# Kernel tuning notes

Measured on AMD Instinct MI355X. Metric: run time of the kernel, lower is better.

Reference implementation:

```python
import jax, jax.numpy as jnp
import numpy as np

# AttentiveErasing hyperparameters (module defaults)
FILL = 0.0
P = 0.5
MIN_FACTOR = 0.0
MAX_FACTOR = 0.5
MIN_H = 4
MIN_W = 4

B, C, H, W = 512, 1, 224, 224


def setup_inputs() -> dict:
    key = jax.random.key(0)
    # x are attention maps in [0,1]; they are used as bernoulli probabilities.
    x = jax.random.uniform(key, (B, C, H, W), dtype=jnp.float32)
    return {"x": x}


def _per_sample_mask(xmap, factor, key):
    # xmap: [H, W] single-channel attention map for one sample
    h_dim, w_dim = xmap.shape
    k_apply, k_h, k_w = jax.random.split(key, 3)
    apply_flag = jax.random.uniform(k_apply) < P  # torch.rand(1) < p

    flat = xmap.reshape(-1)
    c = jnp.argmax(flat)                 # topk(.,1) center
    cy, cx = c // w_dim, c % w_dim
    mx = flat[c]
    mn = jnp.min(flat)
    thr = mx - (mx - mn) * factor
    prop = xmap > thr                    # proposal region

    ridx = jnp.arange(h_dim)
    cidx = jnp.arange(w_dim)
    rows = jnp.any(prop, axis=1)
    cols = jnp.any(prop, axis=0)
    any_prop = jnp.any(prop)             # empty proposals (factor==0) -> torch raises -> skip
    miny = jnp.min(jnp.where(rows, ridx, h_dim))
    maxy = jnp.max(jnp.where(rows, ridx, -1))
    minx = jnp.min(jnp.where(cols, cidx, w_dim))
    maxx = jnp.max(jnp.where(cols, cidx, -1))
    mh2 = (maxy - miny) // 2
    mw2 = (maxx - minx) // 2
    # torch.randint(min, max//2) raises when max//2 <= min -> except: pass -> skip sample
    valid = any_prop & (mh2 > MIN_H) & (mw2 > MIN_W)

    h = MIN_H + (jax.random.uniform(k_h) * jnp.maximum(mh2 - MIN_H, 1)).astype(jnp.int32)
    w = MIN_W + (jax.random.uniform(k_w) * jnp.maximum(mw2 - MIN_W, 1)).astype(jnp.int32)

    h_start = jnp.maximum(cy - h, 0)
    h_end = jnp.minimum(cy + h, w_dim)   # bug preserved: source clamps height with x.size(3)
    w_start = jnp.maximum(cx - w, 0)
    w_end = jnp.minimum(cx + w, w_dim)

    yy = ridx[:, None]
    xx = cidx[None, :]
    # keep proposal iff strictly inside window AND both coords nonzero (y*x > 0 in source)
    erase = (prop & (yy > h_start) & (yy < h_end)
             & (xx > w_start) & (xx < w_end) & (yy > 0) & (xx > 0))
    do = apply_flag & valid
    return jnp.where(do & erase, FILL, 1.0).astype(xmap.dtype)


def _forward(x):
    b = x.shape[0]
    root = jax.random.key(42)
    k_factor, k_samples, k_noise = jax.random.split(root, 3)
    factor = jax.random.uniform(k_factor, minval=MIN_FACTOR, maxval=MAX_FACTOR)
    keys = jax.random.split(k_samples, b)
    mask2d = jax.vmap(lambda xm, k: _per_sample_mask(xm, factor, k))(x[:, 0], keys)
    mask = mask2d[:, None, :, :]          # [B,1,H,W]

    inp = 0.6 * x + 0.2                   # Dropout input; values in [0.2, 0.8]
    keep_prob = jnp.clip(1.0 - jax.lax.stop_gradient(inp), 0.0, 1.0)
    prob_mask = jax.random.bernoulli(k_noise, keep_prob).astype(x.dtype)
    noise = (1.0 - mask) * prob_mask + mask  # region_mask==1 -> keep; ==0 -> bernoulli
    out = inp * noise
    return out, mask


def reference(x):
    return _forward(x)
```

## Files before the change

### kernel.cpp

```cpp
#include <hip/hip_runtime.h>
#include <cstdint>

typedef unsigned int u32;
typedef float vf4 __attribute__((ext_vector_type(4)));

#define TF_R4(a,b,r1,r2,r3,r4) \
  a += b; b = (b<<r1)|(b>>(32-r1)); b ^= a; \
  a += b; b = (b<<r2)|(b>>(32-r2)); b ^= a; \
  a += b; b = (b<<r3)|(b>>(32-r3)); b ^= a; \
  a += b; b = (b<<r4)|(b>>(32-r4)); b ^= a;

__host__ __device__ inline void tf2x32(u32 k0, u32 k1, u32& x0, u32& x1) {
  const u32 k2 = k0 ^ k1 ^ 0x1BD11BDAu;
  u32 a = x0 + k0, b = x1 + k1;
  TF_R4(a,b,13,15,26,6)   a += k1; b += k2 + 1u;
  TF_R4(a,b,17,29,16,24)  a += k2; b += k0 + 2u;
  TF_R4(a,b,13,15,26,6)   a += k0; b += k1 + 3u;
  TF_R4(a,b,17,29,16,24)  a += k1; b += k2 + 4u;
  TF_R4(a,b,13,15,26,6)   a += k2; b += k0 + 5u;
  x0 = a; x1 = b;
}

__host__ __device__ inline float u01(u32 bits) {
  union { u32 u; float f; } c; c.u = (bits >> 9) | 0x3f800000u;
  return c.f - 1.0f;
}
__host__ __device__ inline u32 rbits_scalar(u32 k0, u32 k1) {
  u32 a = 0, b = 0; tf2x32(k0, k1, a, b); return a ^ b;
}

#define BATCH   512
#define HW      224
#define S       50176
#define NTOT    25690112
#define APB     49
#define FSTR    1152

struct SP { float thr; int hs, he, wss, wee, doit; int pad0, pad1; };
struct AMask { unsigned long long m[8]; };

__global__ __launch_bounds__(256) void k_stats(const float* __restrict__ x,
                                               float* __restrict__ fdata,
                                               AMask am) {
  const int bid = blockIdx.x;
  const int b = bid >> 2, q = bid & 3;
  if (!((am.m[b >> 6] >> (b & 63)) & 1ull)) return;

  const int t = threadIdx.x;
  const int lane = t & 63, wv = t >> 6;
  const float* __restrict__ xs = x + (size_t)b * S;
  float* __restrict__ base = fdata + (size_t)b * FSTR;
  const bool act = lane < 56;

  vf4 cmax = (vf4){0.f, 0.f, 0.f, 0.f};
  float amax = -1.f; int aidx = 0x7fffffff; float amin = 2.f;

#pragma unroll
  for (int k = 0; k < 14; ++k) {
    const int r = q * 56 + wv * 14 + k;
    vf4 v = (vf4){-1.f, -1.f, -1.f, -1.f};
    if (act) v = ((const vf4*)(xs + (size_t)r * HW))[lane];
    float rv = fmaxf(fmaxf(v[0], v[1]), fmaxf(v[2], v[3]));
    if (act) {
      cmax[0] = fmaxf(cmax[0], v[0]); cmax[1] = fmaxf(cmax[1], v[1]);
      cmax[2] = fmaxf(cmax[2], v[2]); cmax[3] = fmaxf(cmax[3], v[3]);
      const int fb = r * HW + lane * 4;
      if (v[0] > amax) { amax = v[0]; aidx = fb; }
      if (v[1] > amax) { amax = v[1]; aidx = fb + 1; }
      if (v[2] > amax) { amax = v[2]; aidx = fb + 2; }
      if (v[3] > amax) { amax = v[3]; aidx = fb + 3; }
      amin = fminf(amin, fminf(fminf(v[0], v[1]), fminf(v[2], v[3])));
    }
    for (int off = 32; off; off >>= 1) rv = fmaxf(rv, __shfl_xor(rv, off));
    if (lane == 0) base[r] = rv;
  }
  for (int off = 32; off; off >>= 1) {
    float v2 = __shfl_xor(amax, off);
    int   i2 = __shfl_xor(aidx, off);
    float n2 = __shfl_xor(amin, off);
    if (v2 > amax || (v2 == amax && i2 < aidx)) { amax = v2; aidx = i2; }
    amin = fminf(amin, n2);
  }
  __shared__ vf4 cmw[4][56];
  __shared__ float wmx[4]; __shared__ int wix[4]; __shared__ float wmn[4];
  if (act) cmw[wv][lane] = cmax;
  if (lane == 0) { wmx[wv] = amax; wix[wv] = aidx; wmn[wv] = amin; }
  __syncthreads();
  if (t < 56) {
    vf4 a = cmw[0][t], c1 = cmw[1][t], c2 = cmw[2][t], c3 = cmw[3][t];
    vf4 m;
    m[0] = fmaxf(fmaxf(a[0], c1[0]), fmaxf(c2[0], c3[0]));
    m[1] = fmaxf(fmaxf(a[1], c1[1]), fmaxf(c2[1], c3[1]));
    m[2] = fmaxf(fmaxf(a[2], c1[2]), fmaxf(c2[2], c3[2]));
    m[3] = fmaxf(fmaxf(a[3], c1[3]), fmaxf(c2[3], c3[3]));
    ((vf4*)(base + 224 + q * 224))[t] = m;
  }
  if (t == 0) {
    float mx = wmx[0]; int ix = wix[0]; float mn = wmn[0];
    for (int wI = 1; wI < 4; ++wI) {
      if (wmx[wI] > mx || (wmx[wI] == mx && wix[wI] < ix)) { mx = wmx[wI]; ix = wix[wI]; }
      mn = fminf(mn, wmn[wI]);
    }
    base[1120 + q * 3 + 0] = mx;
    base[1120 + q * 3 + 1] = __int_as_float(ix);
    base[1120 + q * 3 + 2] = mn;
  }
}

__global__ __launch_bounds__(256) void k_box(const float* __restrict__ fdata,
                                             SP* __restrict__ sp,
                                             float factor, u32 ks0, u32 ks1,
                                             AMask am) {
  const int b = blockIdx.x;
  const int t = threadIdx.x;
  const int lane = t & 63, wv = t >> 6;

  if (!((am.m[b >> 6] >> (b & 63)) & 1ull)) {
    if (t == 0) {
      SP p; p.thr = 0.f; p.hs = 0; p.he = 0; p.wss = 0; p.wee = 0;
      p.doit = 0; p.pad0 = 0; p.pad1 = 0;
      sp[b] = p;
    }
    return;
  }

  const float* __restrict__ base = fdata + (size_t)b * FSTR;
  __shared__ float sc_thr; __shared__ int sc_ix;
  __shared__ int r0[4], r1[4], r2[4], r3[4];

  if (t == 0) {
    float mx = -1.f; int ix = 0x7fffffff; float mn = 2.f;
#pragma unroll
    for (int q2 = 0; q2 < 4; ++q2) {
      const float v = base[1120 + q2 * 3 + 0];
      const int   i = __float_as_int(base[1120 + q2 * 3 + 1]);
      const float n = base[1120 + q2 * 3 + 2];
      if (v > mx || (v == mx && i < ix)) { mx = v; ix = i; }
      mn = fminf(mn, n);
    }
    sc_thr = __fsub_rn(mx, __fmul_rn(__fsub_rn(mx, mn), factor));
    sc_ix = ix;
  }
  __syncthreads();
  const float thr = sc_thr;

  int miny = HW, maxy = -1, minx = HW, maxx = -1;
  if (t < HW) {
    if (base[t] > thr) { miny = t; maxy = t; }
    const float c0 = base[224 + t],       c1 = base[224 + 224 + t];
    const float c2 = base[224 + 448 + t], c3 = base[224 + 672 + t];
    if (fmaxf(fmaxf(c0, c1), fmaxf(c2, c3)) > thr) { minx = t; maxx = t; }
  }
  for (int off = 32; off; off >>= 1) {
    miny = min(miny, __shfl_xor(miny, off));
    maxy = max(maxy, __shfl_xor(maxy, off));
    minx = min(minx, __shfl_xor(minx, off));
    maxx = max(maxx, __shfl_xor(maxx, off));
  }
  if (lane == 0) { r0[wv] = miny; r1[wv] = maxy; r2[wv] = minx; r3[wv] = maxx; }
  __syncthreads();
  if (t == 0) {
    int mny = r0[0], mxy = r1[0], mnx = r2[0], mxx = r3[0];
    for (int wI = 1; wI < 4; ++wI) {
      mny = min(mny, r0[wI]); mxy = max(mxy, r1[wI]);
      mnx = min(mnx, r2[wI]); mxx = max(mxx, r3[wI]);
    }
    const bool any = (mxy >= 0);
    const int mh2 = (mxy - mny) / 2;
    const int mw2 = (mxx - mnx) / 2;
    const bool valid = any && (mh2 > 4) && (mw2 > 4);

    u32 kb0 = 0, kb1 = (u32)b; tf2x32(ks0, ks1, kb0, kb1);
    u32 kh0 = 0, kh1 = 1; tf2x32(kb0, kb1, kh0, kh1);
    u32 kw0 = 0, kw1 = 2; tf2x32(kb0, kb1, kw0, kw1);
    const float uh = u01(rbits_scalar(kh0, kh1));
    const float uw = u01(rbits_scalar(kw0, kw1));

    const int cy = sc_ix / HW, cx = sc_ix % HW;
    const int h = 4 + (int)(uh * (float)max(mh2 - 4, 1));
    const int w = 4 + (int)(uw * (float)max(mw2 - 4, 1));
    SP p;
    p.thr = thr;
    p.hs = max(cy - h, 0); p.he = min(cy + h, HW);
    p.wss = max(cx - w, 0); p.wee = min(cx + w, HW);
    p.doit = valid ? 1 : 0;
    p.pad0 = 0; p.pad1 = 0;
    sp[b] = p;
  }
}

__global__ __launch_bounds__(256) void k_apply(const float* __restrict__ x,
                                               const SP* __restrict__ sp,
                                               float* __restrict__ out,
                                               u32 kn0, u32 kn1) {
  const int bid = blockIdx.x;
  const int b   = bid / APB;
  const int i   = (bid % APB) * 256 + threadIdx.x;
  const SP p = sp[b];
  const vf4 vv = ((const vf4*)(x + (size_t)b * S))[i];
  vf4* __restrict__ os = (vf4*)(out + (size_t)b * S);
  vf4* __restrict__ ms = (vf4*)(out + (size_t)NTOT + (size_t)b * S);

  const int base = i * 4;
  const int y = base / HW, x0 = base % HW;
  const bool yin = p.doit && (y > p.hs) && (y < p.he) && (y > 0);
  const u32 eoff = (u32)b * (u32)S;

  vf4 o, m;
  int need = 0;
#pragma unroll
  for (int j = 0; j < 4; ++j) {
    const float val = vv[j];
    const float inp = __fadd_rn(__fmul_rn(0.6f, val), 0.2f);
    const int xx = x0 + j;
    const bool mz = yin && (val > p.thr) && (xx > p.wss) && (xx < p.wee) && (xx > 0);
    m[j] = mz ? 0.0f : 1.0f;
    o[j] = inp;
    if (mz) need |= 1 << j;
  }
  if (need) {
#pragma unroll
    for (int j = 0; j < 4; ++j) {
      if (need & (1 << j)) {
        const float kp = fminf(fmaxf(__fsub_rn(1.0f, o[j]), 0.0f), 1.0f);
        u32 c0 = 0u, c1 = eoff + (u32)(base + j);
        tf2x32(kn0, kn1, c0, c1);
        if (!(u01(c0 ^ c1) < kp)) o[j] = 0.0f;
      }
    }
  }
  __builtin_nontemporal_store(o, &os[i]);
  __builtin_nontemporal_store(m, &ms[i]);
}

extern "C" void kernel_launch(void* const* d_in, const int* in_sizes, int n_in,
                              void* d_out, int out_size, void* d_ws, size_t ws_size,
                              hipStream_t stream) {
  const float* x = (const float*)d_in[0];
  float* out = (float*)d_out;
  SP*    sp    = (SP*)d_ws;
  float* fdata = (float*)((char*)d_ws + 16384);

  u32 kf0 = 0, kf1 = 0; tf2x32(0u, 42u, kf0, kf1);
  u32 ks0 = 0, ks1 = 1; tf2x32(0u, 42u, ks0, ks1);
  u32 kn0 = 0, kn1 = 2; tf2x32(0u, 42u, kn0, kn1);
  float factor = fmaxf(0.0f, u01(rbits_scalar(kf0, kf1)) * 0.5f);

  AMask am;
  for (int i = 0; i < 8; ++i) am.m[i] = 0ull;
  for (int b = 0; b < BATCH; ++b) {
    u32 kb0 = 0, kb1 = (u32)b; tf2x32(ks0, ks1, kb0, kb1);
    u32 ka0 = 0, ka1 = 0; tf2x32(kb0, kb1, ka0, ka1);
    if (u01(rbits_scalar(ka0, ka1)) < 0.5f) am.m[b >> 6] |= 1ull << (b & 63);
  }

  hipLaunchKernelGGL(k_stats, dim3(BATCH * 4), dim3(256), 0, stream,
                     x, fdata, am);
  hipLaunchKernelGGL(k_box,   dim3(BATCH), dim3(256), 0, stream,
                     fdata, sp, factor, ks0, ks1, am);
  hipLaunchKernelGGL(k_apply, dim3(BATCH * APB), dim3(256), 0, stream,
                     x, sp, out, kn0, kn1);
}
```

Measured before the change: 69.78 us.

## Handle non-applied samples in the stats pass and skip them in apply

Samples whose apply flag is false need no Bernoulli draw or box, so their outputs (scaled input and an all-ones mask) are now written by extra blocks in the first kernel, running alongside the stats blocks. The apply kernel returns early for those samples, so the RNG-heavy work only covers the applied half. This spreads the memory traffic across two launches and lets the non-applied writes overlap with the stats reduction. In exchange the first kernel's grid is much larger and has mixed block roles.

```diff
diff --git a/kernel.cpp b/kernel.cpp
--- a/kernel.cpp
+++ b/kernel.cpp
@@ -35,18 +35,42 @@
 #define NTOT    25690112
 #define APB     49
 #define FSTR    1152
+#define NSTATB  2048
 
 struct SP { float thr; int hs, he, wss, wee, doit; int pad0, pad1; };
 struct AMask { unsigned long long m[8]; };
 
-__global__ __launch_bounds__(256) void k_stats(const float* __restrict__ x,
+__device__ __forceinline__ bool applyb(const AMask& am, int b) {
+  return (am.m[b >> 6] >> (b & 63)) & 1ull;
+}
+
+__global__ __launch_bounds__(256) void k_pass1(const float* __restrict__ x,
+                                               float* __restrict__ out,
                                                float* __restrict__ fdata,
                                                AMask am) {
   const int bid = blockIdx.x;
+  const int t = threadIdx.x;
+
+  if (bid >= NSTATB) {
+    const int idx = bid - NSTATB;
+    const int b = idx / APB;
+    if (applyb(am, b)) return;
+    const int i = (idx % APB) * 256 + t;
+    const vf4 v = ((const vf4*)(x + (size_t)b * S))[i];
+    vf4 o;
+    o[0] = __fadd_rn(__fmul_rn(0.6f, v[0]), 0.2f);
+    o[1] = __fadd_rn(__fmul_rn(0.6f, v[1]), 0.2f);
+    o[2] = __fadd_rn(__fmul_rn(0.6f, v[2]), 0.2f);
+    o[3] = __fadd_rn(__fmul_rn(0.6f, v[3]), 0.2f);
+    const vf4 ones = (vf4){1.f, 1.f, 1.f, 1.f};
+    __builtin_nontemporal_store(o,    &((vf4*)(out + (size_t)b * S))[i]);
+    __builtin_nontemporal_store(ones, &((vf4*)(out + (size_t)NTOT + (size_t)b * S))[i]);
+    return;
+  }
+
   const int b = bid >> 2, q = bid & 3;
-  if (!((am.m[b >> 6] >> (b & 63)) & 1ull)) return;
-
-  const int t = threadIdx.x;
+  if (!applyb(am, b)) return;
+
   const int lane = t & 63, wv = t >> 6;
   const float* __restrict__ xs = x + (size_t)b * S;
   float* __restrict__ base = fdata + (size_t)b * FSTR;
@@ -115,7 +139,7 @@
   const int t = threadIdx.x;
   const int lane = t & 63, wv = t >> 6;
 
-  if (!((am.m[b >> 6] >> (b & 63)) & 1ull)) {
+  if (!applyb(am, b)) {
     if (t == 0) {
       SP p; p.thr = 0.f; p.hs = 0; p.he = 0; p.wss = 0; p.wee = 0;
       p.doit = 0; p.pad0 = 0; p.pad1 = 0;
@@ -192,9 +216,11 @@
 __global__ __launch_bounds__(256) void k_apply(const float* __restrict__ x,
                                                const SP* __restrict__ sp,
                                                float* __restrict__ out,
-                                               u32 kn0, u32 kn1) {
+                                               u32 kn0, u32 kn1, AMask am) {
   const int bid = blockIdx.x;
   const int b   = bid / APB;
+  if (!applyb(am, b)) return;
+
   const int i   = (bid % APB) * 256 + threadIdx.x;
   const SP p = sp[b];
   const vf4 vv = ((const vf4*)(x + (size_t)b * S))[i];
@@ -254,10 +280,10 @@
     if (u01(rbits_scalar(ka0, ka1)) < 0.5f) am.m[b >> 6] |= 1ull << (b & 63);
   }
 
-  hipLaunchKernelGGL(k_stats, dim3(BATCH * 4), dim3(256), 0, stream,
-                     x, fdata, am);
+  hipLaunchKernelGGL(k_pass1, dim3(NSTATB + BATCH * APB), dim3(256), 0, stream,
+                     x, out, fdata, am);
   hipLaunchKernelGGL(k_box,   dim3(BATCH), dim3(256), 0, stream,
                      fdata, sp, factor, ks0, ks1, am);
   hipLaunchKernelGGL(k_apply, dim3(BATCH * APB), dim3(256), 0, stream,
-                     x, sp, out, kn0, kn1);
-}
+                     x, sp, out, kn0, kn1, am);
+}
```

New measurement: 63.00 us. -9.7%, faster.
